# Performance work log

Measured on AMD Instinct MI355X. Metric: run time of the kernel, lower is better.

Reference implementation:

```python
import jax, jax.numpy as jnp
import numpy as np

C = 512
GROUPS = 8
EPS = 1e-5


def setup_inputs() -> dict:
    key = jax.random.key(0)
    ks = jax.random.split(key, 11)
    B, H, W = 8, 64, 64
    x = jax.random.normal(ks[0], (B, C, H, W), dtype=jnp.float32)
    s = 1.0 / np.sqrt(C)
    return {
        "x": x,
        "gn_w": jnp.ones((C,), jnp.float32),
        "gn_b": jnp.zeros((C,), jnp.float32),
        "wq": jax.random.normal(ks[1], (C, C), jnp.float32) * s,
        "bq": jnp.zeros((C,), jnp.float32),
        "wk": jax.random.normal(ks[2], (C, C), jnp.float32) * s,
        "bk": jnp.zeros((C,), jnp.float32),
        "wv": jax.random.normal(ks[3], (C, C), jnp.float32) * s,
        "bv": jnp.zeros((C,), jnp.float32),
        "wo": jax.random.normal(ks[4], (C, C), jnp.float32) * s,
        "bo": jnp.zeros((C,), jnp.float32),
    }


def _group_norm(x, w, b):
    # x: [B, C, H, W], 8 groups over channel dim
    B, Ch, H, W = x.shape
    xg = x.reshape(B, GROUPS, Ch // GROUPS, H, W)
    mu = jnp.mean(xg, axis=(2, 3, 4), keepdims=True)
    var = jnp.var(xg, axis=(2, 3, 4), keepdims=True)
    xn = ((xg - mu) * jax.lax.rsqrt(var + EPS)).reshape(B, Ch, H, W)
    return xn * w[None, :, None, None] + b[None, :, None, None]


def reference(x, gn_w, gn_b, wq, bq, wk, bk, wv, bv, wo, bo):
    B, Ch, H, W = x.shape
    h = _group_norm(x, gn_w, gn_b)
    # [B, N, C] tokens, N = H*W
    h = h.reshape(B, Ch, H * W).transpose(0, 2, 1)
    q = jnp.einsum('bnc,dc->bnd', h, wq) + bq
    k = jnp.einsum('bnc,dc->bnd', h, wk) + bk
    v = jnp.einsum('bnc,dc->bnd', h, wv) + bv
    scores = jnp.einsum('bnd,bmd->bnm', q, k) / jnp.sqrt(jnp.float32(Ch))
    attn = jax.nn.softmax(scores, axis=-1)
    out = jnp.einsum('bnm,bmd->bnd', attn, v)
    out = jnp.einsum('bnd,ed->bne', out, wo) + bo
    out = out.transpose(0, 2, 1).reshape(B, Ch, H, W)
    return x + out
```

## Files before the change

### kernel.cpp

```cpp
#include <hip/hip_runtime.h>
#include <hip/hip_bf16.h>
#include <stdint.h>

typedef __hip_bfloat16 bf16;
typedef unsigned short u16;
typedef unsigned int u32;
using short8  = __attribute__((ext_vector_type(8))) short;
using short4v = __attribute__((ext_vector_type(4))) short;
using floatx4 = __attribute__((ext_vector_type(4))) float;
using uintx4  = __attribute__((ext_vector_type(4))) u32;

#define SCALE_L2E 0.06375872f

__device__ __forceinline__ float b2f(u16 u) {
  union { u32 i; float f; } v; v.i = ((u32)u) << 16; return v.f;
}
__device__ __forceinline__ u16 f2b(float f) {
  union { float f; u32 i; } v; v.f = f;
  u32 r = v.i + 0x7fffu + ((v.i >> 16) & 1u);
  return (u16)(r >> 16);
}

__device__ __forceinline__ void gl2lds16(const void* g, void* l) {
  __builtin_amdgcn_global_load_lds(
      (const __attribute__((address_space(1))) void*)g,
      (__attribute__((address_space(3))) void*)l,
      16, 0, 0);
}

__global__ __launch_bounds__(256)
void cvt_weights(const float* __restrict__ w0, const float* __restrict__ w1,
                 const float* __restrict__ w2, const float* __restrict__ w3,
                 u16* __restrict__ o0, u16* __restrict__ o1,
                 u16* __restrict__ o2, u16* __restrict__ o3)
{
  const float* w = blockIdx.y == 0 ? w0 : blockIdx.y == 1 ? w1 : blockIdx.y == 2 ? w2 : w3;
  u16* o = blockIdx.y == 0 ? o0 : blockIdx.y == 1 ? o1 : blockIdx.y == 2 ? o2 : o3;
  const int i = (blockIdx.x * 256 + threadIdx.x) * 4;
  floatx4 v = *(const floatx4*)(w + i);
  short4v p;
#pragma unroll
  for (int j = 0; j < 4; j++) p[j] = (short)f2b(v[j]);
  *(short4v*)(o + i) = p;
}

__global__ __launch_bounds__(256)
void gn_stats(const float* __restrict__ x, float* __restrict__ gmean, float* __restrict__ grstd)
{
  const int g = blockIdx.x, b = blockIdx.y;
  const float* base = x + ((long)(b * 512 + g * 64)) * 4096;
  const int t = threadIdx.x;
  float s = 0.f, ss = 0.f;
  for (int i = 0; i < 256; i++) {
    floatx4 v = *(const floatx4*)(base + i * 1024 + t * 4);
#pragma unroll
    for (int j = 0; j < 4; j++) { s += v[j]; ss += v[j] * v[j]; }
  }
  for (int off = 1; off < 64; off <<= 1) {
    s  += __shfl_xor(s, off, 64);
    ss += __shfl_xor(ss, off, 64);
  }
  __shared__ float as_[4], ass_[4];
  if ((t & 63) == 0) { as_[t >> 6] = s; ass_[t >> 6] = ss; }
  __syncthreads();
  if (t == 0) {
    float S1 = as_[0] + as_[1] + as_[2] + as_[3];
    float S2 = ass_[0] + ass_[1] + ass_[2] + ass_[3];
    const float inv = 1.0f / 262144.0f;
    float mu = S1 * inv;
    float var = S2 * inv - mu * mu;
    gmean[b * 8 + g] = mu;
    grstd[b * 8 + g] = rsqrtf(var + 1e-5f);
  }
}

__global__ __launch_bounds__(256)
void gn_apply(const float* __restrict__ x, const float* __restrict__ gw, const float* __restrict__ gb,
              const float* __restrict__ gmean, const float* __restrict__ grstd,
              bf16* __restrict__ h)
{
  const int b = blockIdx.z;
  const int c0 = blockIdx.y * 64;
  const int p0 = blockIdx.x * 64;
  const int t = threadIdx.x;
  const int c = c0 + (t & 63);
  const int g = c >> 6;
  const float mu = gmean[b * 8 + g], rs = grstd[b * 8 + g];
  const float wv = gw[c];
  const float bv = gb[c];
  const float a = rs * wv;
  const float bb = bv - mu * rs * wv;
  const float* xp = x + ((long)(b * 512 + c)) * 4096;
  u16* hp = (u16*)h + ((long)b * 4096) * 512 + c;
  const int pbase = p0 + (t >> 6);
#pragma unroll
  for (int i = 0; i < 16; i++) {
    int p = pbase + i * 4;
    float xv = xp[p];
    hp[(long)p * 512] = f2b(xv * a + bb);
  }
}

constexpr int BM = 128, BN = 128, BK = 32;

template<int MODE>
__global__ __launch_bounds__(256)
void gemm_bt(const bf16* __restrict__ Ag, long sA,
             const bf16* __restrict__ Bg, long sB,
             const float* __restrict__ bias,
             const float* __restrict__ bias2,
             const float* __restrict__ bias3,
             const float* __restrict__ resid, long sR,
             bf16* __restrict__ Og, long sO, long sO2,
             int M, int N, int K)
{
  __shared__ u16 As[2][BM * BK];
  __shared__ u16 Bs[2][BN * BK];
  const int t = threadIdx.x;
  const int bz = blockIdx.x;
  const int bm = blockIdx.y;
  const int bn = blockIdx.z;

  const u16* A = (const u16*)Ag + (long)bz * sA;
  const u16* B = (const u16*)Bg + (long)bz * sB;

  const int lane = t & 63, w = t >> 6;

  const int rs_ = w * 16 + (lane >> 2);
  const int seg = ((lane & 3) ^ ((rs_ >> 1) & 3)) * 8;
  const long aOff  = (long)(bm * BM + rs_) * K + seg;
  const long bOff  = (long)(bn * BN + rs_) * K + seg;
  const long aOff2 = aOff + 64L * K;
  const long bOff2 = bOff + 64L * K;
  const int wofs = w * 1024;

  const int wm = (w >> 1) * 64, wn = (w & 1) * 64;
  const int lc = lane & 15, quad = lane >> 4;

  int aoffs[4], boffs[4];
#pragma unroll
  for (int i = 0; i < 4; i++) {
    const int Ra = wm + i * 16 + lc;
    const int Rb = wn + i * 16 + lc;
    aoffs[i] = Ra * 64 + ((quad ^ ((Ra >> 1) & 3)) * 16);
    boffs[i] = Rb * 64 + ((quad ^ ((Rb >> 1) & 3)) * 16);
  }

  floatx4 acc[4][4];
#pragma unroll
  for (int i = 0; i < 4; i++)
#pragma unroll
    for (int j = 0; j < 4; j++) acc[i][j] = (floatx4)0.f;

  auto stage = [&](int buf, int kk) {
    char* aw = (char*)&As[buf][0] + wofs;
    char* bw = (char*)&Bs[buf][0] + wofs;
    gl2lds16(A + aOff  + kk, aw);
    gl2lds16(A + aOff2 + kk, aw + 4096);
    gl2lds16(B + bOff  + kk, bw);
    gl2lds16(B + bOff2 + kk, bw + 4096);
  };

  stage(0, 0);
  int cur = 0;
  for (int kk = 0; kk < K; kk += BK) {
    __syncthreads();
    if (kk + BK < K) stage(cur ^ 1, kk + BK);
    const char* Ac = (const char*)&As[cur][0];
    const char* Bc = (const char*)&Bs[cur][0];
    short8 af[4], bfr[4];
#pragma unroll
    for (int i = 0; i < 4; i++) af[i]  = *(const short8*)(Ac + aoffs[i]);
#pragma unroll
    for (int j = 0; j < 4; j++) bfr[j] = *(const short8*)(Bc + boffs[j]);
#pragma unroll
    for (int i = 0; i < 4; i++)
#pragma unroll
      for (int j = 0; j < 4; j++)
        acc[i][j] = __builtin_amdgcn_mfma_f32_16x16x32_bf16(af[i], bfr[j], acc[i][j], 0, 0, 0);
    cur ^= 1;
  }

#pragma unroll
  for (int i = 0; i < 4; i++) {
    const int gm0 = bm * BM + wm + i * 16 + quad * 4;
#pragma unroll
    for (int j = 0; j < 4; j++) {
      const int gn = bn * BN + wn + j * 16 + lc;
      floatx4 a = acc[i][j];
      if (MODE == 4) {
        float* Of = (float*)Og + (long)bz * sO;
        const float bv = bias[gn];
        const float* Rz = resid + (long)bz * sR;
        const floatx4 rv = *(const floatx4*)&Rz[(long)gn * M + gm0];
        floatx4 p;
#pragma unroll
        for (int rg = 0; rg < 4; rg++) p[rg] = a[rg] + bv + rv[rg];
        *(floatx4*)&Of[(long)gn * M + gm0] = p;
      } else {
        const int nt = gn >> 9;
        const int col = gn & 511;
        const float bvv = (nt == 0 ? bias : nt == 1 ? bias2 : bias3)[col];
        u16* Ou = (u16*)Og + (long)nt * sO2 + (long)bz * sO;
        if (nt < 2) {
#pragma unroll
          for (int rg = 0; rg < 4; rg++)
            Ou[(long)(gm0 + rg) * 512 + col] = f2b(a[rg] + bvv);
        } else {
          short4v p;
#pragma unroll
          for (int rg = 0; rg < 4; rg++) p[rg] = (short)f2b(a[rg] + bvv);
          *(short4v*)&Ou[(long)col * M + gm0] = p;
        }
      }
    }
  }
}

#define COMPUTE_SLAB(S, BUF)                                                \
  {                                                                         \
    _Pragma("unroll")                                                       \
    for (int ks = 0; ks < 4; ks++) {                                        \
      short8 vf[2], pf[4];                                                  \
      _Pragma("unroll")                                                     \
      for (int mf = 0; mf < 2; mf++) {                                      \
        const int r = wr * 32 + mf * 16 + lc;                               \
        vf[mf] = *(const short8*)((const char*)&vt_s[BUF][0] +              \
                   r * 256 + (((ks * 4 + quad) ^ (r & 7)) * 16));           \
      }                                                                     \
      _Pragma("unroll")                                                     \
      for (int nf = 0; nf < 4; nf++) {                                      \
        const int r = wc * 64 + nf * 16 + lc;                               \
        pf[nf] = *(const short8*)((const char*)p_s +                        \
                   r * 256 + (((ks * 4 + quad) ^ (r & 7)) * 16));           \
      }                                                                     \
      _Pragma("unroll")                                                     \
      for (int mf = 0; mf < 2; mf++)                                        \
        _Pragma("unroll")                                                   \
        for (int nf = 0; nf < 4; nf++)                                      \
          acc_o[S][mf][nf] = __builtin_amdgcn_mfma_f32_16x16x32_bf16(       \
              vf[mf], pf[nf], acc_o[S][mf][nf], 0, 0, 0);                   \
    }                                                                       \
  }

__global__ __launch_bounds__(512, 2)
void fused_attn(const bf16* __restrict__ qg, const bf16* __restrict__ kg,
                const bf16* __restrict__ vtg, bf16* __restrict__ og)
{
  __shared__ u16 qk_s[2][2][128 * 32];
  __shared__ u16 vt_s[2][128 * 128];
  __shared__ u16 p_s[128 * 128];
  __shared__ float rsum_s[4][128];

  const int t = threadIdx.x;
  const int lane = t & 63, w = t >> 6;
  const int lc = lane & 15, quad = lane >> 4;
  const int wr = w >> 1, wc = w & 1;
  const int z = blockIdx.x, qt = blockIdx.y;
  const long zoff = (long)z * (4096L * 512);
  const u16* q_z  = (const u16*)qg + zoff;
  const u16* k_z  = (const u16*)kg + zoff;
  const u16* vt_z = (const u16*)vtg + zoff;
  u16* o_z = (u16*)og + zoff;

  const int srow = t >> 2;
  const int sseg = ((t & 3) ^ ((srow >> 1) & 3)) * 8;
  const u16* qsrc  = q_z + (long)(qt * 128 + srow) * 512 + sseg;
  const u16* ksrcC = k_z + (long)srow * 512 + sseg;
  const int vrow = t >> 4;
  const int vseg = ((t & 15) ^ (vrow & 7)) * 8;
  const u16* vsrcC = vt_z + (long)vrow * 4096 + vseg;

  const int ldsbase = w * 1024;

  int koff[2], qoff[4];
#pragma unroll
  for (int mf = 0; mf < 2; mf++) {
    const int r = wr * 32 + mf * 16 + lc;
    koff[mf] = r * 64 + ((quad ^ ((r >> 1) & 3)) * 16);
  }
#pragma unroll
  for (int nf = 0; nf < 4; nf++) {
    const int r = wc * 64 + nf * 16 + lc;
    qoff[nf] = r * 64 + ((quad ^ ((r >> 1) & 3)) * 16);
  }

  auto stage_qk = [&](int buf, int ds) {
    char* base = (char*)&qk_s[buf][0][0] + ldsbase;
    gl2lds16(qsrc  + ds * 32, base);
    gl2lds16(ksrcC + ds * 32, base + 8192);
  };
  auto stage_vt = [&](int buf, int slab) {
    char* base = (char*)&vt_s[buf][0] + ldsbase;
    const u16* vs = vsrcC + (long)slab * (128L * 4096);
#pragma unroll
    for (int i = 0; i < 4; i++)
      gl2lds16(vs + (long)i * (32L * 4096), base + i * 8192);
  };

  floatx4 acc_o[4][2][4];
#pragma unroll
  for (int s = 0; s < 4; s++)
#pragma unroll
    for (int mf = 0; mf < 2; mf++)
#pragma unroll
      for (int nf = 0; nf < 4; nf++) acc_o[s][mf][nf] = (floatx4)0.f;
  float rsum[4] = {0.f, 0.f, 0.f, 0.f};

  for (int ck = 0; ck < 32; ++ck) {
    floatx4 acc_s[2][4];
#pragma unroll
    for (int mf = 0; mf < 2; mf++)
#pragma unroll
      for (int nf = 0; nf < 4; nf++) acc_s[mf][nf] = (floatx4)0.f;

    stage_qk(0, 0);
#pragma unroll 2
    for (int ds = 0; ds < 16; ++ds) {
      __syncthreads();
      if (ds < 15) stage_qk((ds + 1) & 1, ds + 1);
      else         stage_vt(0, 0);
      const int b = ds & 1;
      const char* Kc = (const char*)&qk_s[b][1][0];
      const char* Qc = (const char*)&qk_s[b][0][0];
      short8 kf[2], qf[4];
#pragma unroll
      for (int mf = 0; mf < 2; mf++) kf[mf] = *(const short8*)(Kc + koff[mf]);
#pragma unroll
      for (int nf = 0; nf < 4; nf++) qf[nf] = *(const short8*)(Qc + qoff[nf]);
#pragma unroll
      for (int mf = 0; mf < 2; mf++)
#pragma unroll
        for (int nf = 0; nf < 4; nf++)
          acc_s[mf][nf] = __builtin_amdgcn_mfma_f32_16x16x32_bf16(kf[mf], qf[nf], acc_s[mf][nf], 0, 0, 0);
    }

#pragma unroll
    for (int mf = 0; mf < 2; mf++)
#pragma unroll
      for (int nf = 0; nf < 4; nf++) {
        floatx4 a = acc_s[mf][nf];
        float p0 = exp2f(a[0] * SCALE_L2E);
        float p1 = exp2f(a[1] * SCALE_L2E);
        float p2 = exp2f(a[2] * SCALE_L2E);
        float p3 = exp2f(a[3] * SCALE_L2E);
        rsum[nf] += (p0 + p1) + (p2 + p3);
        short4v pk;
        pk[0] = (short)f2b(p0); pk[1] = (short)f2b(p1);
        pk[2] = (short)f2b(p2); pk[3] = (short)f2b(p3);
        const int key0 = wr * 32 + mf * 16 + quad * 4;
        const int qq = wc * 64 + nf * 16 + lc;
        *(short4v*)((char*)p_s + qq * 256 + ((key0 * 2) ^ ((qq & 7) << 4))) = pk;
      }

    __syncthreads();
    stage_vt(1, 1);
    COMPUTE_SLAB(0, 0)
    __syncthreads();
    stage_vt(0, 2);
    COMPUTE_SLAB(1, 1)
    __syncthreads();
    stage_vt(1, 3);
    COMPUTE_SLAB(2, 0)
    __syncthreads();
    COMPUTE_SLAB(3, 1)

    ksrcC += 128 * 512;
    vsrcC += 128;
  }

#pragma unroll
  for (int nf = 0; nf < 4; nf++) {
    float s = rsum[nf];
    s += __shfl_xor(s, 16, 64);
    s += __shfl_xor(s, 32, 64);
    if (lane < 16) rsum_s[wr][wc * 64 + nf * 16 + lane] = s;
  }
  __syncthreads();

#pragma unroll
  for (int s = 0; s < 4; s++)
#pragma unroll
    for (int mf = 0; mf < 2; mf++)
#pragma unroll
      for (int nf = 0; nf < 4; nf++) {
        const int qq = wc * 64 + nf * 16 + lc;
        const float tot = (rsum_s[0][qq] + rsum_s[1][qq]) + (rsum_s[2][qq] + rsum_s[3][qq]);
        const float r = 1.0f / tot;
        floatx4 a = acc_o[s][mf][nf];
        short4v ov;
#pragma unroll
        for (int rg = 0; rg < 4; rg++) ov[rg] = (short)f2b(a[rg] * r);
        const int d0 = s * 128 + wr * 32 + mf * 16 + quad * 4;
        *(short4v*)&o_z[(long)(qt * 128 + qq) * 512 + d0] = ov;
      }
}

extern "C" void kernel_launch(void* const* d_in, const int* in_sizes, int n_in,
                              void* d_out, int out_size, void* d_ws, size_t ws_size,
                              hipStream_t stream)
{
  const float* x  = (const float*)d_in[0];
  const float* gw = (const float*)d_in[1];
  const float* gb = (const float*)d_in[2];
  const float* wq = (const float*)d_in[3];
  const float* bq = (const float*)d_in[4];
  const float* wk = (const float*)d_in[5];
  const float* bk = (const float*)d_in[6];
  const float* wv = (const float*)d_in[7];
  const float* bv = (const float*)d_in[8];
  const float* wo = (const float*)d_in[9];
  const float* bo = (const float*)d_in[10];

  const long PB = (long)4096 * 512;

  auto need = [&](long nb) -> size_t {
    return (size_t)(4 * 262144 * 2 + nb * PB * 2 * 4 + 8192);
  };
  long nB = 1;
  const long cand_nB[4] = {8, 4, 2, 1};
  for (int i = 0; i < 4; i++)
    if (need(cand_nB[i]) <= ws_size) { nB = cand_nB[i]; break; }

  char* ws = (char*)d_ws;
  u16*   wqb  = (u16*)ws;
  u16*   wkb  = wqb + 262144;
  u16*   wvb  = wkb + 262144;
  u16*   wob  = wvb + 262144;
  bf16*  h    = (bf16*)(wob + 262144);
  bf16*  q    = h  + nB * PB;
  bf16*  k    = q  + nB * PB;
  bf16*  vT   = k  + nB * PB;
  bf16*  o    = h;
  float* gm   = (float*)(vT + nB * PB);
  float* gr   = gm + 64;

  cvt_weights<<<dim3(256, 4), 256, 0, stream>>>(wq, wk, wv, wo, wqb, wkb, wvb, wob);
  gn_stats<<<dim3(8, 8), 256, 0, stream>>>(x, gm, gr);

  for (long b0 = 0; b0 < 8; b0 += nB) {
    const int gs = (int)nB;

    gn_apply<<<dim3(64, 8, gs), 256, 0, stream>>>(x + b0 * PB, gw, gb, gm + b0 * 8, gr + b0 * 8, h);

    gemm_bt<5><<<dim3(gs, 32, 12), 256, 0, stream>>>(
        h, PB, (bf16*)wqb, 0, bq, bk, bv, nullptr, 0,
        q, PB, nB * PB, 4096, 1536, 512);

    fused_attn<<<dim3(gs, 32), 512, 0, stream>>>(q, k, vT, o);

    gemm_bt<4><<<dim3(gs, 32, 4), 256, 0, stream>>>(
        o, PB, (bf16*)wob, 0, bo, nullptr, nullptr,
        x + b0 * PB, PB, (bf16*)((float*)d_out + b0 * PB), PB, 0, 4096, 512, 512);
  }
}
```

Baseline: 767.9 us.

## Triple-buffer QK staging with explicit vmcnt waits and MFMA priority

Moves the Q/K LDS staging from double to triple buffering. It prefetches two slabs ahead, including the first slabs of the next key chunk during the PV phase, and replaces __syncthreads with explicit partial vmcnt waits plus raw barriers so async global-to-LDS loads stay in flight across barriers. It also raises wave priority around the MFMA blocks and fully unrolls the QK loop. The goal is to hide global load latency and barrier stalls, at the cost of extra LDS and fragile hand-counted waitcnt values that could race if the counts are wrong.

```diff
diff --git a/kernel.cpp b/kernel.cpp
--- a/kernel.cpp
+++ b/kernel.cpp
@@ -11,6 +11,9 @@
 using uintx4  = __attribute__((ext_vector_type(4))) u32;
 
 #define SCALE_L2E 0.06375872f
+
+#define SWAITL(vm) asm volatile("s_waitcnt vmcnt(" #vm ") lgkmcnt(0)" ::: "memory")
+#define SBARC() do { __builtin_amdgcn_s_barrier(); asm volatile("" ::: "memory"); } while (0)
 
 __device__ __forceinline__ float b2f(u16 u) {
   union { u32 i; float f; } v; v.i = ((u32)u) << 16; return v.f;
@@ -219,6 +222,7 @@
 
 #define COMPUTE_SLAB(S, BUF)                                                \
   {                                                                         \
+    __builtin_amdgcn_s_setprio(1);                                          \
     _Pragma("unroll")                                                       \
     for (int ks = 0; ks < 4; ks++) {                                        \
       short8 vf[2], pf[4];                                                  \
@@ -241,13 +245,14 @@
           acc_o[S][mf][nf] = __builtin_amdgcn_mfma_f32_16x16x32_bf16(       \
               vf[mf], pf[nf], acc_o[S][mf][nf], 0, 0, 0);                   \
     }                                                                       \
+    __builtin_amdgcn_s_setprio(0);                                          \
   }
 
 __global__ __launch_bounds__(512, 2)
 void fused_attn(const bf16* __restrict__ qg, const bf16* __restrict__ kg,
                 const bf16* __restrict__ vtg, bf16* __restrict__ og)
 {
-  __shared__ u16 qk_s[2][2][128 * 32];
+  __shared__ u16 qk_s[3][2][128 * 32];
   __shared__ u16 vt_s[2][128 * 128];
   __shared__ u16 p_s[128 * 128];
   __shared__ float rsum_s[4][128];
@@ -285,10 +290,10 @@
     qoff[nf] = r * 64 + ((quad ^ ((r >> 1) & 3)) * 16);
   }
 
-  auto stage_qk = [&](int buf, int ds) {
+  auto stage_qk = [&](int buf, int ds, const u16* ks) {
     char* base = (char*)&qk_s[buf][0][0] + ldsbase;
-    gl2lds16(qsrc  + ds * 32, base);
-    gl2lds16(ksrcC + ds * 32, base + 8192);
+    gl2lds16(qsrc + ds * 32, base);
+    gl2lds16(ks   + ds * 32, base + 8192);
   };
   auto stage_vt = [&](int buf, int slab) {
     char* base = (char*)&vt_s[buf][0] + ldsbase;
@@ -307,32 +312,39 @@
       for (int nf = 0; nf < 4; nf++) acc_o[s][mf][nf] = (floatx4)0.f;
   float rsum[4] = {0.f, 0.f, 0.f, 0.f};
 
+  stage_qk(0, 0, ksrcC);
+  stage_qk(1, 1, ksrcC);
+
   for (int ck = 0; ck < 32; ++ck) {
+    const u16* ksrcN = ksrcC + 128 * 512;
+
     floatx4 acc_s[2][4];
 #pragma unroll
     for (int mf = 0; mf < 2; mf++)
 #pragma unroll
       for (int nf = 0; nf < 4; nf++) acc_s[mf][nf] = (floatx4)0.f;
 
-    stage_qk(0, 0);
-#pragma unroll 2
+#pragma unroll
     for (int ds = 0; ds < 16; ++ds) {
-      __syncthreads();
-      if (ds < 15) stage_qk((ds + 1) & 1, ds + 1);
-      else         stage_vt(0, 0);
-      const int b = ds & 1;
-      const char* Kc = (const char*)&qk_s[b][1][0];
-      const char* Qc = (const char*)&qk_s[b][0][0];
+      if (ds == 15) { SWAITL(4); } else { SWAITL(2); }
+      SBARC();
+      if (ds < 14)       stage_qk((ds + 2) % 3, ds + 2, ksrcC);
+      else if (ds == 14) stage_vt(0, 0);
+      else               stage_vt(1, 1);
+      const char* Kc = (const char*)&qk_s[ds % 3][1][0];
+      const char* Qc = (const char*)&qk_s[ds % 3][0][0];
       short8 kf[2], qf[4];
 #pragma unroll
       for (int mf = 0; mf < 2; mf++) kf[mf] = *(const short8*)(Kc + koff[mf]);
 #pragma unroll
       for (int nf = 0; nf < 4; nf++) qf[nf] = *(const short8*)(Qc + qoff[nf]);
+      __builtin_amdgcn_s_setprio(1);
 #pragma unroll
       for (int mf = 0; mf < 2; mf++)
 #pragma unroll
         for (int nf = 0; nf < 4; nf++)
           acc_s[mf][nf] = __builtin_amdgcn_mfma_f32_16x16x32_bf16(kf[mf], qf[nf], acc_s[mf][nf], 0, 0, 0);
+      __builtin_amdgcn_s_setprio(0);
     }
 
 #pragma unroll
@@ -353,19 +365,24 @@
         *(short4v*)((char*)p_s + qq * 256 + ((key0 * 2) ^ ((qq & 7) << 4))) = pk;
       }
 
-    __syncthreads();
-    stage_vt(1, 1);
+    SWAITL(4);
+    SBARC();
     COMPUTE_SLAB(0, 0)
-    __syncthreads();
+    SWAITL(0);
+    SBARC();
     stage_vt(0, 2);
+    stage_qk(0, 0, ksrcN);
     COMPUTE_SLAB(1, 1)
-    __syncthreads();
+    SWAITL(2);
+    SBARC();
     stage_vt(1, 3);
+    stage_qk(1, 1, ksrcN);
     COMPUTE_SLAB(2, 0)
-    __syncthreads();
+    SWAITL(2);
+    SBARC();
     COMPUTE_SLAB(3, 1)
 
-    ksrcC += 128 * 512;
+    ksrcC = ksrcN;
     vsrcC += 128;
   }
 
```

Result: no change. 776.6 us (+1.1%).

## Halve attention query tile to 64 rows and raise occupancy to four blocks

Applied to the files above, without the earlier changes.

The fused attention kernel now handles 64 query rows per block instead of 128. It shrinks LDS buffers and accumulator registers, uses a new wave layout, splits the PV product into eight 64-wide d-slabs, and sets launch bounds to 4 blocks per CU. It also wraps the MFMA sections in s_setprio and swaps the grid order so query tiles come first. The aim is more blocks per CU and more latency hiding. The cost is that K and V are reloaded twice as often, and there are more barriers per key chunk.

```diff
diff --git a/kernel.cpp b/kernel.cpp
--- a/kernel.cpp
+++ b/kernel.cpp
@@ -219,44 +219,45 @@
 
 #define COMPUTE_SLAB(S, BUF)                                                \
   {                                                                         \
+    __builtin_amdgcn_s_setprio(1);                                          \
     _Pragma("unroll")                                                       \
     for (int ks = 0; ks < 4; ks++) {                                        \
-      short8 vf[2], pf[4];                                                  \
+      short8 vf[2], pf;                                                     \
       _Pragma("unroll")                                                     \
       for (int mf = 0; mf < 2; mf++) {                                      \
-        const int r = wr * 32 + mf * 16 + lc;                               \
+        const int r = wd * 32 + mf * 16 + lc;                               \
         vf[mf] = *(const short8*)((const char*)&vt_s[BUF][0] +              \
                    r * 256 + (((ks * 4 + quad) ^ (r & 7)) * 16));           \
       }                                                                     \
-      _Pragma("unroll")                                                     \
-      for (int nf = 0; nf < 4; nf++) {                                      \
-        const int r = wc * 64 + nf * 16 + lc;                               \
-        pf[nf] = *(const short8*)((const char*)p_s +                        \
+      {                                                                     \
+        const int r = wqp * 16 + lc;                                        \
+        pf = *(const short8*)((const char*)p_s +                            \
                    r * 256 + (((ks * 4 + quad) ^ (r & 7)) * 16));           \
       }                                                                     \
       _Pragma("unroll")                                                     \
       for (int mf = 0; mf < 2; mf++)                                        \
-        _Pragma("unroll")                                                   \
-        for (int nf = 0; nf < 4; nf++)                                      \
-          acc_o[S][mf][nf] = __builtin_amdgcn_mfma_f32_16x16x32_bf16(       \
-              vf[mf], pf[nf], acc_o[S][mf][nf], 0, 0, 0);                   \
+        acc_o[S][mf] = __builtin_amdgcn_mfma_f32_16x16x32_bf16(             \
+            vf[mf], pf, acc_o[S][mf], 0, 0, 0);                             \
     }                                                                       \
-  }
-
-__global__ __launch_bounds__(512, 2)
+    __builtin_amdgcn_s_setprio(0);                                          \
+  }
+
+__global__ __launch_bounds__(512, 4)
 void fused_attn(const bf16* __restrict__ qg, const bf16* __restrict__ kg,
                 const bf16* __restrict__ vtg, bf16* __restrict__ og)
 {
-  __shared__ u16 qk_s[2][2][128 * 32];
-  __shared__ u16 vt_s[2][128 * 128];
-  __shared__ u16 p_s[128 * 128];
-  __shared__ float rsum_s[4][128];
+  __shared__ u16 q_s[2][64 * 32];
+  __shared__ u16 k_s[2][128 * 32];
+  __shared__ u16 vt_s[2][64 * 128];
+  __shared__ u16 p_s[64 * 128];
+  __shared__ float rsum_s[4][64];
 
   const int t = threadIdx.x;
   const int lane = t & 63, w = t >> 6;
   const int lc = lane & 15, quad = lane >> 4;
-  const int wr = w >> 1, wc = w & 1;
-  const int z = blockIdx.x, qt = blockIdx.y;
+  const int wk = w >> 1, wq2 = w & 1;
+  const int wd = w >> 2, wqp = w & 3;
+  const int qt = blockIdx.x, z = blockIdx.y;
   const long zoff = (long)z * (4096L * 512);
   const u16* q_z  = (const u16*)qg + zoff;
   const u16* k_z  = (const u16*)kg + zoff;
@@ -265,54 +266,48 @@
 
   const int srow = t >> 2;
   const int sseg = ((t & 3) ^ ((srow >> 1) & 3)) * 8;
-  const u16* qsrc  = q_z + (long)(qt * 128 + srow) * 512 + sseg;
+  const u16* qsrc  = q_z + (long)(qt * 64 + (srow & 63)) * 512 + sseg;
   const u16* ksrcC = k_z + (long)srow * 512 + sseg;
-  const int vrow = t >> 4;
-  const int vseg = ((t & 15) ^ (vrow & 7)) * 8;
-  const u16* vsrcC = vt_z + (long)vrow * 4096 + vseg;
+  const int vrow0 = t >> 4;
+  const u16* vsrcC = vt_z + (long)vrow0 * 4096 + (((t & 15) ^ (vrow0 & 7)) * 8);
 
   const int ldsbase = w * 1024;
 
-  int koff[2], qoff[4];
+  int koff[2], qoff[2];
 #pragma unroll
   for (int mf = 0; mf < 2; mf++) {
-    const int r = wr * 32 + mf * 16 + lc;
+    const int r = wk * 32 + mf * 16 + lc;
     koff[mf] = r * 64 + ((quad ^ ((r >> 1) & 3)) * 16);
   }
 #pragma unroll
-  for (int nf = 0; nf < 4; nf++) {
-    const int r = wc * 64 + nf * 16 + lc;
+  for (int nf = 0; nf < 2; nf++) {
+    const int r = wq2 * 32 + nf * 16 + lc;
     qoff[nf] = r * 64 + ((quad ^ ((r >> 1) & 3)) * 16);
   }
 
   auto stage_qk = [&](int buf, int ds) {
-    char* base = (char*)&qk_s[buf][0][0] + ldsbase;
-    gl2lds16(qsrc  + ds * 32, base);
-    gl2lds16(ksrcC + ds * 32, base + 8192);
+    gl2lds16(ksrcC + ds * 32, (char*)&k_s[buf][0] + ldsbase);
+    if (t < 256) gl2lds16(qsrc + ds * 32, (char*)&q_s[buf][0] + ldsbase);
   };
   auto stage_vt = [&](int buf, int slab) {
     char* base = (char*)&vt_s[buf][0] + ldsbase;
-    const u16* vs = vsrcC + (long)slab * (128L * 4096);
-#pragma unroll
-    for (int i = 0; i < 4; i++)
-      gl2lds16(vs + (long)i * (32L * 4096), base + i * 8192);
+    gl2lds16(vsrcC + (long)(slab * 64)      * 4096, base);
+    gl2lds16(vsrcC + (long)(slab * 64 + 32) * 4096, base + 8192);
   };
 
-  floatx4 acc_o[4][2][4];
-#pragma unroll
-  for (int s = 0; s < 4; s++)
+  floatx4 acc_o[8][2];
+#pragma unroll
+  for (int s = 0; s < 8; s++)
+#pragma unroll
+    for (int mf = 0; mf < 2; mf++) acc_o[s][mf] = (floatx4)0.f;
+  float rsum[2] = {0.f, 0.f};
+
+  for (int ck = 0; ck < 32; ++ck) {
+    floatx4 acc_s[2][2];
 #pragma unroll
     for (int mf = 0; mf < 2; mf++)
 #pragma unroll
-      for (int nf = 0; nf < 4; nf++) acc_o[s][mf][nf] = (floatx4)0.f;
-  float rsum[4] = {0.f, 0.f, 0.f, 0.f};
-
-  for (int ck = 0; ck < 32; ++ck) {
-    floatx4 acc_s[2][4];
-#pragma unroll
-    for (int mf = 0; mf < 2; mf++)
-#pragma unroll
-      for (int nf = 0; nf < 4; nf++) acc_s[mf][nf] = (floatx4)0.f;
+      for (int nf = 0; nf < 2; nf++) acc_s[mf][nf] = (floatx4)0.f;
 
     stage_qk(0, 0);
 #pragma unroll 2
@@ -321,24 +316,26 @@
       if (ds < 15) stage_qk((ds + 1) & 1, ds + 1);
       else         stage_vt(0, 0);
       const int b = ds & 1;
-      const char* Kc = (const char*)&qk_s[b][1][0];
-      const char* Qc = (const char*)&qk_s[b][0][0];
-      short8 kf[2], qf[4];
+      const char* Kc = (const char*)&k_s[b][0];
+      const char* Qc = (const char*)&q_s[b][0];
+      short8 kf[2], qf[2];
 #pragma unroll
       for (int mf = 0; mf < 2; mf++) kf[mf] = *(const short8*)(Kc + koff[mf]);
 #pragma unroll
-      for (int nf = 0; nf < 4; nf++) qf[nf] = *(const short8*)(Qc + qoff[nf]);
+      for (int nf = 0; nf < 2; nf++) qf[nf] = *(const short8*)(Qc + qoff[nf]);
+      __builtin_amdgcn_s_setprio(1);
 #pragma unroll
       for (int mf = 0; mf < 2; mf++)
 #pragma unroll
-        for (int nf = 0; nf < 4; nf++)
+        for (int nf = 0; nf < 2; nf++)
           acc_s[mf][nf] = __builtin_amdgcn_mfma_f32_16x16x32_bf16(kf[mf], qf[nf], acc_s[mf][nf], 0, 0, 0);
+      __builtin_amdgcn_s_setprio(0);
     }
 
 #pragma unroll
     for (int mf = 0; mf < 2; mf++)
 #pragma unroll
-      for (int nf = 0; nf < 4; nf++) {
+      for (int nf = 0; nf < 2; nf++) {
         floatx4 a = acc_s[mf][nf];
         float p0 = exp2f(a[0] * SCALE_L2E);
         float p1 = exp2f(a[1] * SCALE_L2E);
@@ -348,8 +345,8 @@
         short4v pk;
         pk[0] = (short)f2b(p0); pk[1] = (short)f2b(p1);
         pk[2] = (short)f2b(p2); pk[3] = (short)f2b(p3);
-        const int key0 = wr * 32 + mf * 16 + quad * 4;
-        const int qq = wc * 64 + nf * 16 + lc;
+        const int key0 = wk * 32 + mf * 16 + quad * 4;
+        const int qq = wq2 * 32 + nf * 16 + lc;
         *(short4v*)((char*)p_s + qq * 256 + ((key0 * 2) ^ ((qq & 7) << 4))) = pk;
       }
 
@@ -363,37 +360,50 @@
     stage_vt(1, 3);
     COMPUTE_SLAB(2, 0)
     __syncthreads();
+    stage_vt(0, 4);
     COMPUTE_SLAB(3, 1)
+    __syncthreads();
+    stage_vt(1, 5);
+    COMPUTE_SLAB(4, 0)
+    __syncthreads();
+    stage_vt(0, 6);
+    COMPUTE_SLAB(5, 1)
+    __syncthreads();
+    stage_vt(1, 7);
+    COMPUTE_SLAB(6, 0)
+    __syncthreads();
+    COMPUTE_SLAB(7, 1)
 
     ksrcC += 128 * 512;
     vsrcC += 128;
   }
 
 #pragma unroll
-  for (int nf = 0; nf < 4; nf++) {
+  for (int nf = 0; nf < 2; nf++) {
     float s = rsum[nf];
     s += __shfl_xor(s, 16, 64);
     s += __shfl_xor(s, 32, 64);
-    if (lane < 16) rsum_s[wr][wc * 64 + nf * 16 + lane] = s;
+    if (lane < 16) rsum_s[wk][wq2 * 32 + nf * 16 + lane] = s;
   }
   __syncthreads();
 
-#pragma unroll
-  for (int s = 0; s < 4; s++)
-#pragma unroll
-    for (int mf = 0; mf < 2; mf++)
-#pragma unroll
-      for (int nf = 0; nf < 4; nf++) {
-        const int qq = wc * 64 + nf * 16 + lc;
-        const float tot = (rsum_s[0][qq] + rsum_s[1][qq]) + (rsum_s[2][qq] + rsum_s[3][qq]);
-        const float r = 1.0f / tot;
-        floatx4 a = acc_o[s][mf][nf];
+  {
+    const int qq = wqp * 16 + lc;
+    const float tot = (rsum_s[0][qq] + rsum_s[1][qq]) + (rsum_s[2][qq] + rsum_s[3][qq]);
+    const float r = 1.0f / tot;
+    u16* orow = &o_z[(long)(qt * 64 + qq) * 512];
+#pragma unroll
+    for (int s = 0; s < 8; s++)
+#pragma unroll
+      for (int mf = 0; mf < 2; mf++) {
+        floatx4 a = acc_o[s][mf];
         short4v ov;
 #pragma unroll
         for (int rg = 0; rg < 4; rg++) ov[rg] = (short)f2b(a[rg] * r);
-        const int d0 = s * 128 + wr * 32 + mf * 16 + quad * 4;
-        *(short4v*)&o_z[(long)(qt * 128 + qq) * 512 + d0] = ov;
+        const int d0 = s * 64 + wd * 32 + mf * 16 + quad * 4;
+        *(short4v*)&orow[d0] = ov;
       }
+  }
 }
 
 extern "C" void kernel_launch(void* const* d_in, const int* in_sizes, int n_in,
@@ -447,7 +457,7 @@
         h, PB, (bf16*)wqb, 0, bq, bk, bv, nullptr, 0,
         q, PB, nB * PB, 4096, 1536, 512);
 
-    fused_attn<<<dim3(gs, 32), 512, 0, stream>>>(q, k, vT, o);
+    fused_attn<<<dim3(64, gs), 512, 0, stream>>>(q, k, vT, o);
 
     gemm_bt<4><<<dim3(gs, 32, 4), 256, 0, stream>>>(
         o, PB, (bf16*)wob, 0, bo, nullptr, nullptr,
```

Measured after the change: 818.3 us. +6.6%, slower.
